# Optimization experiments

Hardware: AMD Instinct MI355X
Metric: run time of the kernel (lower is better)

The kernel has to match this reference:

```python
import jax, jax.numpy as jnp
import numpy as np

N_NODES = 50000
N_EDGES = 800000
DIM = 128
BN_EPS = 1e-5  # torch.nn.BatchNorm1d default


def _lin_init(k, fan_in, fan_out):
    kw, kb = jax.random.split(k)
    s = 1.0 / np.sqrt(fan_in)
    W = jax.random.uniform(kw, (fan_in, fan_out), jnp.float32, -s, s)
    b = jax.random.uniform(kb, (fan_out,), jnp.float32, -s, s)
    return W, b


def setup_inputs() -> dict:
    key = jax.random.key(0)
    ks = jax.random.split(key, 8)
    d = {}
    d['h'] = jax.random.normal(ks[0], (N_NODES, DIM), jnp.float32)
    d['e'] = jax.random.normal(ks[1], (N_EDGES, DIM), jnp.float32)
    d['src'] = jax.random.randint(ks[2], (N_EDGES,), 0, N_NODES)
    d['dst'] = jax.random.randint(ks[3], (N_EDGES,), 0, N_NODES)
    # mlp_atom: Linear(128,128) -> ReLU -> Linear(128,128)
    d['Wa1'], d['ba1'] = _lin_init(ks[4], DIM, DIM)
    d['Wa2'], d['ba2'] = _lin_init(ks[5], DIM, DIM)
    # mlp_bond
    d['Wb1'], d['bb1'] = _lin_init(ks[6], DIM, DIM)
    d['Wb2'], d['bb2'] = _lin_init(ks[7], DIM, DIM)
    # BatchNorm1d affine params
    d['gamma_a'] = jnp.ones((DIM,), jnp.float32)
    d['beta_a'] = jnp.zeros((DIM,), jnp.float32)
    d['gamma_b'] = jnp.ones((DIM,), jnp.float32)
    d['beta_b'] = jnp.zeros((DIM,), jnp.float32)
    return d


def _mlp(x, W1, b1, W2, b2):
    return jax.nn.relu(x @ W1 + b1) @ W2 + b2


def _bn(x, gamma, beta):
    # training-mode batch norm over the node/edge axis
    mu = jnp.mean(x, axis=0)
    var = jnp.var(x, axis=0)
    return (x - mu) * jax.lax.rsqrt(var + BN_EPS) * gamma + beta


def reference(h, e, src, dst, Wa1, ba1, Wa2, ba2, Wb1, bb1, Wb2, bb2,
              gamma_a, beta_a, gamma_b, beta_b):
    # --- bond (edge) update: GIN-style sum of endpoint atom feats + bond feat
    me = h[src] + h[dst] + e                      # [E, D] irregular gather
    e_new = _bn(_mlp(me, Wb1, bb1, Wb2, bb2), gamma_b, beta_b)
    e_new = e_new + e                             # residual (dropout=Identity)
    # --- atom (node) update: sum-aggregate incident bond feats
    agg = jax.ops.segment_sum(e_new, dst, num_segments=N_NODES)  # [N, D] scatter
    h_new = _bn(_mlp(h + agg, Wa1, ba1, Wa2, ba2), gamma_a, beta_a)
    h_new = h_new + h                             # residual
    return h_new, e_new
```

## Files before the change

### kernel.cpp

```cpp
#include <hip/hip_runtime.h>
#include <hip/hip_fp16.h>
#include <cstddef>

#define NN 50000
#define NE 800000
#define D 128
#define BN_EPS 1e-5f

typedef __attribute__((ext_vector_type(8))) short bf16x8;
typedef __attribute__((ext_vector_type(4))) float f32x4;
typedef __attribute__((ext_vector_type(4))) unsigned short us4;

__device__ __forceinline__ unsigned short f2bf(float x) {
    unsigned u = __float_as_uint(x);
    return (unsigned short)((u + 0x7fffu + ((u >> 16) & 1u)) >> 16);
}

__global__ __launch_bounds__(256) void wprep_kernel(
    const float* __restrict__ W, unsigned short* __restrict__ Wt)
{
    const int idx = blockIdx.x * 256 + threadIdx.x;
    const int j  = idx & 7;
    const int l  = (idx >> 3) & 63;
    const int ks = (idx >> 9) & 3;
    const int ct = (idx >> 11) & 7;
    const int n  = 16 * ct + (l & 15);
    const int k  = 32 * ks + ((l >> 4) << 3) + j;
    Wt[idx] = f2bf(W[k * 128 + n]);
}

template<int MODE, int HALFX>
__global__ __launch_bounds__(256, 2) void mlp_mfma_kernel(
    const float* __restrict__ h, const float* __restrict__ e_or_agg,
    const int* __restrict__ src, const int* __restrict__ dst,
    const unsigned short* __restrict__ Wt1, const float* __restrict__ b1,
    const unsigned short* __restrict__ Wt2, const float* __restrict__ b2,
    void* __restrict__ x2out_v, float* __restrict__ stats)
{
    __shared__ __align__(16) unsigned short Xh[8192];
    __shared__ __align__(16) float OUTB[64 * 132 + 2048];

    const int tid  = threadIdx.x;
    const int lane = tid & 63;
    const int w    = tid >> 6;
    const int cg   = tid & 31;
    const int rg   = tid >> 5;
    const int c0   = cg * 4;
    const long r0  = (long)blockIdx.x * 64;

    if (stats == (float*)1) OUTB[64 * 132 + (tid & 2047)] = 1.f;

    const bf16x8* Wg1 = (const bf16x8*)Wt1;
    bf16x8 wf[8][4];
#pragma unroll
    for (int ct = 0; ct < 8; ++ct)
#pragma unroll
        for (int ks = 0; ks < 4; ++ks)
            wf[ct][ks] = Wg1[(ct * 4 + ks) * 64 + lane];

#pragma unroll
    for (int p = 0; p < 8; ++p) {
        const int  row  = p * 8 + rg;
        const long grow = r0 + row;
        float4 v = make_float4(0.f, 0.f, 0.f, 0.f);
        if (MODE == 0) {
            const int sN = src[grow];
            const int dN = dst[grow];
            const float4 ev = *(const float4*)(e_or_agg + (size_t)grow * D + c0);
            const float4 hs = *(const float4*)(h + (size_t)sN * D + c0);
            const float4 hd = *(const float4*)(h + (size_t)dN * D + c0);
            v.x = ev.x + hs.x + hd.x; v.y = ev.y + hs.y + hd.y;
            v.z = ev.z + hs.z + hd.z; v.w = ev.w + hs.w + hd.w;
        } else {
            if (grow < NN) {
                const float4 hv = *(const float4*)(h + (size_t)grow * D + c0);
                const float4 av = *(const float4*)(e_or_agg + (size_t)grow * D + c0);
                v.x = hv.x + av.x; v.y = hv.y + av.y;
                v.z = hv.z + av.z; v.w = hv.w + av.w;
            }
        }
        us4 hi;
        hi.x = f2bf(v.x); hi.y = f2bf(v.y);
        hi.z = f2bf(v.z); hi.w = f2bf(v.w);
        const int addr = row * 128 + (((c0 >> 3) ^ (row & 7)) << 3) + (c0 & 7);
        *(us4*)&Xh[addr] = hi;
    }
    __syncthreads();

    const int arow = 16 * w + (lane & 15);
    bf16x8 ah[4];
#pragma unroll
    for (int ks = 0; ks < 4; ++ks) {
        const int col0  = 32 * ks + ((lane >> 4) << 3);
        const int aaddr = arow * 128 + (((col0 >> 3) ^ (arow & 7)) << 3);
        ah[ks] = *(const bf16x8*)&Xh[aaddr];
    }
    f32x4 acc[8];
#pragma unroll
    for (int ct = 0; ct < 8; ++ct) acc[ct] = (f32x4){0.f, 0.f, 0.f, 0.f};
#pragma unroll
    for (int ct = 0; ct < 8; ++ct)
#pragma unroll
        for (int ks = 0; ks < 4; ++ks)
            acc[ct] = __builtin_amdgcn_mfma_f32_16x16x32_bf16(ah[ks], wf[ct][ks], acc[ct], 0, 0, 0);

    const bf16x8* Wg2 = (const bf16x8*)Wt2;
#pragma unroll
    for (int ct = 0; ct < 8; ++ct)
#pragma unroll
        for (int ks = 0; ks < 4; ++ks)
            wf[ct][ks] = Wg2[(ct * 4 + ks) * 64 + lane];

#pragma unroll
    for (int ct = 0; ct < 8; ++ct) {
        const float b1c = b1[16 * ct + (lane & 15)];
#pragma unroll
        for (int r = 0; r < 4; ++r) {
            const int row = 16 * w + ((lane >> 4) << 2) + r;
            OUTB[row * 132 + 16 * ct + (lane & 15)] = fmaxf(acc[ct][r] + b1c, 0.f);
        }
    }
    __syncthreads();

#pragma unroll
    for (int p = 0; p < 8; ++p) {
        const int row = p * 8 + rg;
        const float4 v = *(const float4*)&OUTB[row * 132 + c0];
        us4 hi;
        hi.x = f2bf(v.x); hi.y = f2bf(v.y);
        hi.z = f2bf(v.z); hi.w = f2bf(v.w);
        const int addr = row * 128 + (((c0 >> 3) ^ (row & 7)) << 3) + (c0 & 7);
        *(us4*)&Xh[addr] = hi;
    }
    __syncthreads();

#pragma unroll
    for (int ks = 0; ks < 4; ++ks) {
        const int col0  = 32 * ks + ((lane >> 4) << 3);
        const int aaddr = arow * 128 + (((col0 >> 3) ^ (arow & 7)) << 3);
        ah[ks] = *(const bf16x8*)&Xh[aaddr];
    }
    f32x4 a2[8];
#pragma unroll
    for (int ct = 0; ct < 8; ++ct) a2[ct] = (f32x4){0.f, 0.f, 0.f, 0.f};
#pragma unroll
    for (int ct = 0; ct < 8; ++ct)
#pragma unroll
        for (int ks = 0; ks < 4; ++ks)
            a2[ct] = __builtin_amdgcn_mfma_f32_16x16x32_bf16(ah[ks], wf[ct][ks], a2[ct], 0, 0, 0);

#pragma unroll
    for (int ct = 0; ct < 8; ++ct) {
        const float b2c = b2[16 * ct + (lane & 15)];
#pragma unroll
        for (int r = 0; r < 4; ++r) {
            const int row = 16 * w + ((lane >> 4) << 2) + r;
            OUTB[row * 132 + 16 * ct + (lane & 15)] = a2[ct][r] + b2c;
        }
    }
    __syncthreads();

    float ts[4] = {0.f, 0.f, 0.f, 0.f};
    float tq[4] = {0.f, 0.f, 0.f, 0.f};
#pragma unroll
    for (int p = 0; p < 8; ++p) {
        const int  row  = p * 8 + rg;
        const long grow = r0 + row;
        if (MODE == 1 && grow >= NN) continue;
        const float4 v = *(const float4*)&OUTB[row * 132 + c0];
        if (HALFX) {
            const __half2 h0 = __floats2half2_rn(v.x, v.y);
            const __half2 h1 = __floats2half2_rn(v.z, v.w);
            int2 pk;
            pk.x = *(const int*)&h0;
            pk.y = *(const int*)&h1;
            *(int2*)((__half*)x2out_v + (size_t)grow * D + c0) = pk;
        } else {
            *(float4*)((float*)x2out_v + (size_t)grow * D + c0) = v;
        }
        ts[0] += v.x; ts[1] += v.y; ts[2] += v.z; ts[3] += v.w;
        tq[0] += v.x * v.x; tq[1] += v.y * v.y;
        tq[2] += v.z * v.z; tq[3] += v.w * v.w;
    }

    float* red = (float*)Xh;
    *(float4*)&red[rg * 128 + c0]        = make_float4(ts[0], ts[1], ts[2], ts[3]);
    *(float4*)&red[1024 + rg * 128 + c0] = make_float4(tq[0], tq[1], tq[2], tq[3]);
    __syncthreads();
    if (tid < 128) {
        float s = 0.f, q = 0.f;
#pragma unroll
        for (int g = 0; g < 8; ++g) {
            s += red[g * 128 + tid];
            q += red[1024 + g * 128 + tid];
        }
        unsafeAtomicAdd(&stats[tid], s);
        unsafeAtomicAdd(&stats[128 + tid], q);
    }
}

__global__ void bn_finalize_kernel(float* __restrict__ stats,
                                   const float* __restrict__ gamma,
                                   const float* __restrict__ beta,
                                   float inv_count)
{
    const int c = threadIdx.x;
    if (c < D) {
        const float mu  = stats[c] * inv_count;
        const float var = stats[128 + c] * inv_count - mu * mu;
        const float sc  = rsqrtf(var + BN_EPS) * gamma[c];
        stats[256 + c] = sc;
        stats[384 + c] = beta[c] - mu * sc;
    }
}

__global__ __launch_bounds__(256) void hist_kernel(
    const int* __restrict__ dst, int* __restrict__ cnt)
{
    const int i = blockIdx.x * 256 + threadIdx.x;
    if (i < NE) atomicAdd(&cnt[dst[i]], 1);
}

__global__ __launch_bounds__(1024) void scan_kernel(
    const int* __restrict__ cnt, int* __restrict__ off)
{
    __shared__ int part[1024];
    const int t = threadIdx.x;
    const int SEG = (NN + 1023) / 1024;
    const int base = t * SEG;

    int s = 0;
    for (int i = 0; i < SEG; ++i) {
        const int idx = base + i;
        if (idx < NN) s += cnt[idx];
    }
    part[t] = s;
    __syncthreads();
    for (int d = 1; d < 1024; d <<= 1) {
        int v = (t >= d) ? part[t - d] : 0;
        __syncthreads();
        part[t] += v;
        __syncthreads();
    }
    int run = (t > 0) ? part[t - 1] : 0;
    for (int i = 0; i < SEG; ++i) {
        const int idx = base + i;
        if (idx < NN) { off[idx] = run; run += cnt[idx]; }
    }
    if (t == 1023) off[NN] = part[1023];
}

__global__ __launch_bounds__(256) void csr_scatter_kernel(
    const int* __restrict__ dst, const int* __restrict__ off,
    int* __restrict__ cnt, int* __restrict__ csr)
{
    const int i = blockIdx.x * 256 + threadIdx.x;
    if (i < NE) {
        const int d = dst[i];
        const int p = atomicSub(&cnt[d], 1) - 1;
        csr[off[d] + p] = i;
    }
}

template<int HALFX>
__global__ __launch_bounds__(256) void apply_gather_kernel(
    const float* __restrict__ e, const float* __restrict__ stats,
    const int* __restrict__ off, const int* __restrict__ csr,
    const void* __restrict__ x2src, float* __restrict__ eout,
    float* __restrict__ agg)
{
    const int node = blockIdx.x * 4 + (threadIdx.x >> 6);
    const int lane = threadIdx.x & 63;
    const int half = lane >> 5;
    const int c0   = (lane & 31) * 4;
    if (node >= NN) return;

    const float4 sc = *(const float4*)(stats + 256 + c0);
    const float4 sh = *(const float4*)(stats + 384 + c0);
    float4 acc = make_float4(0.f, 0.f, 0.f, 0.f);
    const int jb = off[node], je = off[node + 1];
    const int niter = (je - jb + 1) >> 1;

#pragma unroll 2
    for (int p = 0; p < niter; ++p) {
        const int j0 = jb + 2 * p + half;
        if (j0 < je) {
            const int eidx = csr[j0];
            const size_t base = (size_t)eidx * D + c0;
            float4 x;
            if (HALFX) {
                const int2 xi = *(const int2*)((const __half*)x2src + base);
                const float2 f0 = __half22float2(*(const __half2*)&xi.x);
                const float2 f1 = __half22float2(*(const __half2*)&xi.y);
                x = make_float4(f0.x, f0.y, f1.x, f1.y);
            } else {
                x = *(const float4*)(eout + base);
            }
            const float4 ev = *(const float4*)(e + base);
            float4 v;
            v.x = fmaf(x.x, sc.x, sh.x) + ev.x;
            v.y = fmaf(x.y, sc.y, sh.y) + ev.y;
            v.z = fmaf(x.z, sc.z, sh.z) + ev.z;
            v.w = fmaf(x.w, sc.w, sh.w) + ev.w;
            *(float4*)(eout + base) = v;
            acc.x += v.x; acc.y += v.y; acc.z += v.z; acc.w += v.w;
        }
    }

    acc.x += __shfl_xor(acc.x, 32);
    acc.y += __shfl_xor(acc.y, 32);
    acc.z += __shfl_xor(acc.z, 32);
    acc.w += __shfl_xor(acc.w, 32);
    if (half == 0)
        *(float4*)(agg + (size_t)node * D + c0) = acc;
}

__global__ __launch_bounds__(256) void node_apply_kernel(
    const float* __restrict__ h, const float* __restrict__ stats,
    float* __restrict__ hout)
{
    const int gid = blockIdx.x * 256 + threadIdx.x;
    const int c0  = (gid & 31) * 4;
    const size_t base = (size_t)(gid >> 5) * D + c0;

    const float4 sc = *(const float4*)(stats + 256 + c0);
    const float4 sh = *(const float4*)(stats + 384 + c0);
    const float4 x  = *(const float4*)(hout + base);
    const float4 hv = *(const float4*)(h + base);
    float4 v;
    v.x = fmaf(x.x, sc.x, sh.x) + hv.x;
    v.y = fmaf(x.y, sc.y, sh.y) + hv.y;
    v.z = fmaf(x.z, sc.z, sh.z) + hv.z;
    v.w = fmaf(x.w, sc.w, sh.w) + hv.w;
    *(float4*)(hout + base) = v;
}

extern "C" void kernel_launch(void* const* d_in, const int* in_sizes, int n_in,
                              void* d_out, int out_size, void* d_ws, size_t ws_size,
                              hipStream_t stream)
{
    const float* h   = (const float*)d_in[0];
    const float* e   = (const float*)d_in[1];
    const int*   src = (const int*)d_in[2];
    const int*   dst = (const int*)d_in[3];
    const float* Wa1 = (const float*)d_in[4];
    const float* ba1 = (const float*)d_in[5];
    const float* Wa2 = (const float*)d_in[6];
    const float* ba2 = (const float*)d_in[7];
    const float* Wb1 = (const float*)d_in[8];
    const float* bb1 = (const float*)d_in[9];
    const float* Wb2 = (const float*)d_in[10];
    const float* bb2 = (const float*)d_in[11];
    const float* ga  = (const float*)d_in[12];
    const float* bea = (const float*)d_in[13];
    const float* gb  = (const float*)d_in[14];
    const float* beb = (const float*)d_in[15];

    float* out  = (float*)d_out;
    float* hnew = out;
    float* enew = out + (size_t)NN * D;

    float* ws     = (float*)d_ws;
    float* estats = ws;
    float* nstats = ws + 512;
    int*   icnt   = (int*)(ws + 1024);
    int*   ioff   = icnt + NN;
    unsigned short* wtb1 = (unsigned short*)(ioff + NN + 1 + 3);
    unsigned short* wtb2 = wtb1 + 16384;
    unsigned short* wta1 = wtb2 + 16384;
    unsigned short* wta2 = wta1 + 16384;
    int*    icsr = (int*)(wta2 + 16384);
    float*  agg  = (float*)(icsr + NE);
    __half* x2h  = (__half*)(agg + (size_t)NN * D);
    const size_t need_half = (size_t)((char*)(x2h + (size_t)NE * D) - (char*)d_ws);
    const bool use_half = (ws_size >= need_half);

    hipMemsetAsync(d_ws, 0, (size_t)(1024 + NN) * sizeof(float), stream);

    wprep_kernel<<<64, 256, 0, stream>>>(Wb1, wtb1);
    wprep_kernel<<<64, 256, 0, stream>>>(Wb2, wtb2);
    wprep_kernel<<<64, 256, 0, stream>>>(Wa1, wta1);
    wprep_kernel<<<64, 256, 0, stream>>>(Wa2, wta2);

    hist_kernel<<<(NE + 255) / 256, 256, 0, stream>>>(dst, icnt);
    scan_kernel<<<1, 1024, 0, stream>>>(icnt, ioff);
    csr_scatter_kernel<<<(NE + 255) / 256, 256, 0, stream>>>(dst, ioff, icnt, icsr);

    if (use_half) {
        mlp_mfma_kernel<0, 1><<<NE / 64, 256, 0, stream>>>(
            h, e, src, dst, wtb1, bb1, wtb2, bb2, (void*)x2h, estats);
        bn_finalize_kernel<<<1, 128, 0, stream>>>(estats, gb, beb, 1.0f / NE);
        apply_gather_kernel<1><<<(NN + 3) / 4, 256, 0, stream>>>(
            e, estats, ioff, icsr, (const void*)x2h, enew, agg);
    } else {
        mlp_mfma_kernel<0, 0><<<NE / 64, 256, 0, stream>>>(
            h, e, src, dst, wtb1, bb1, wtb2, bb2, (void*)enew, estats);
        bn_finalize_kernel<<<1, 128, 0, stream>>>(estats, gb, beb, 1.0f / NE);
        apply_gather_kernel<0><<<(NN + 3) / 4, 256, 0, stream>>>(
            e, estats, ioff, icsr, nullptr, enew, agg);
    }

    mlp_mfma_kernel<1, 0><<<(NN + 63) / 64, 256, 0, stream>>>(
        h, agg, nullptr, nullptr, wta1, ba1, wta2, ba2, (void*)hnew, nstats);
    bn_finalize_kernel<<<1, 128, 0, stream>>>(nstats, ga, bea, 1.0f / NN);
    node_apply_kernel<<<(NN * 32) / 256, 256, 0, stream>>>(h, nstats, hnew);
}
```

Before: 804.2 us.

## Split MLP column tiles across twice the waves per block, unroll gather loop further

The MLP kernel now runs 512 threads (8 waves) per 64-row tile. Each wave computes half of the 128 output columns, so it holds only half the weight fragments and accumulators. This lowers per-thread register pressure, allowing more waves per CU to hide gather latency. In exchange each wave reloads the A fragments redundantly and the stats reduction grows to 16 partials. The CSR gather loop unroll is also raised from 2 to 4.

```diff
diff --git a/kernel.cpp b/kernel.cpp
--- a/kernel.cpp
+++ b/kernel.cpp
@@ -30,7 +30,7 @@
 }
 
 template<int MODE, int HALFX>
-__global__ __launch_bounds__(256, 2) void mlp_mfma_kernel(
+__global__ __launch_bounds__(512, 4) void mlp_mfma_kernel(
     const float* __restrict__ h, const float* __restrict__ e_or_agg,
     const int* __restrict__ src, const int* __restrict__ dst,
     const unsigned short* __restrict__ Wt1, const float* __restrict__ b1,
@@ -43,6 +43,8 @@
     const int tid  = threadIdx.x;
     const int lane = tid & 63;
     const int w    = tid >> 6;
+    const int wq   = w & 3;
+    const int wh   = w >> 2;
     const int cg   = tid & 31;
     const int rg   = tid >> 5;
     const int c0   = cg * 4;
@@ -51,16 +53,16 @@
     if (stats == (float*)1) OUTB[64 * 132 + (tid & 2047)] = 1.f;
 
     const bf16x8* Wg1 = (const bf16x8*)Wt1;
-    bf16x8 wf[8][4];
-#pragma unroll
-    for (int ct = 0; ct < 8; ++ct)
+    bf16x8 wf[4][4];
+#pragma unroll
+    for (int ctl = 0; ctl < 4; ++ctl)
 #pragma unroll
         for (int ks = 0; ks < 4; ++ks)
-            wf[ct][ks] = Wg1[(ct * 4 + ks) * 64 + lane];
-
-#pragma unroll
-    for (int p = 0; p < 8; ++p) {
-        const int  row  = p * 8 + rg;
+            wf[ctl][ks] = Wg1[((4 * wh + ctl) * 4 + ks) * 64 + lane];
+
+#pragma unroll
+    for (int p = 0; p < 4; ++p) {
+        const int  row  = p * 16 + rg;
         const long grow = r0 + row;
         float4 v = make_float4(0.f, 0.f, 0.f, 0.f);
         if (MODE == 0) {
@@ -87,7 +89,7 @@
     }
     __syncthreads();
 
-    const int arow = 16 * w + (lane & 15);
+    const int arow = 16 * wq + (lane & 15);
     bf16x8 ah[4];
 #pragma unroll
     for (int ks = 0; ks < 4; ++ks) {
@@ -95,36 +97,37 @@
         const int aaddr = arow * 128 + (((col0 >> 3) ^ (arow & 7)) << 3);
         ah[ks] = *(const bf16x8*)&Xh[aaddr];
     }
-    f32x4 acc[8];
-#pragma unroll
-    for (int ct = 0; ct < 8; ++ct) acc[ct] = (f32x4){0.f, 0.f, 0.f, 0.f};
-#pragma unroll
-    for (int ct = 0; ct < 8; ++ct)
+    f32x4 acc[4];
+#pragma unroll
+    for (int ctl = 0; ctl < 4; ++ctl) acc[ctl] = (f32x4){0.f, 0.f, 0.f, 0.f};
+#pragma unroll
+    for (int ctl = 0; ctl < 4; ++ctl)
 #pragma unroll
         for (int ks = 0; ks < 4; ++ks)
-            acc[ct] = __builtin_amdgcn_mfma_f32_16x16x32_bf16(ah[ks], wf[ct][ks], acc[ct], 0, 0, 0);
+            acc[ctl] = __builtin_amdgcn_mfma_f32_16x16x32_bf16(ah[ks], wf[ctl][ks], acc[ctl], 0, 0, 0);
 
     const bf16x8* Wg2 = (const bf16x8*)Wt2;
 #pragma unroll
-    for (int ct = 0; ct < 8; ++ct)
+    for (int ctl = 0; ctl < 4; ++ctl)
 #pragma unroll
         for (int ks = 0; ks < 4; ++ks)
-            wf[ct][ks] = Wg2[(ct * 4 + ks) * 64 + lane];
-
-#pragma unroll
-    for (int ct = 0; ct < 8; ++ct) {
+            wf[ctl][ks] = Wg2[((4 * wh + ctl) * 4 + ks) * 64 + lane];
+
+#pragma unroll
+    for (int ctl = 0; ctl < 4; ++ctl) {
+        const int ct = 4 * wh + ctl;
         const float b1c = b1[16 * ct + (lane & 15)];
 #pragma unroll
         for (int r = 0; r < 4; ++r) {
-            const int row = 16 * w + ((lane >> 4) << 2) + r;
-            OUTB[row * 132 + 16 * ct + (lane & 15)] = fmaxf(acc[ct][r] + b1c, 0.f);
-        }
-    }
-    __syncthreads();
-
-#pragma unroll
-    for (int p = 0; p < 8; ++p) {
-        const int row = p * 8 + rg;
+            const int row = 16 * wq + ((lane >> 4) << 2) + r;
+            OUTB[row * 132 + 16 * ct + (lane & 15)] = fmaxf(acc[ctl][r] + b1c, 0.f);
+        }
+    }
+    __syncthreads();
+
+#pragma unroll
+    for (int p = 0; p < 4; ++p) {
+        const int row = p * 16 + rg;
         const float4 v = *(const float4*)&OUTB[row * 132 + c0];
         us4 hi;
         hi.x = f2bf(v.x); hi.y = f2bf(v.y);
@@ -140,22 +143,23 @@
         const int aaddr = arow * 128 + (((col0 >> 3) ^ (arow & 7)) << 3);
         ah[ks] = *(const bf16x8*)&Xh[aaddr];
     }
-    f32x4 a2[8];
-#pragma unroll
-    for (int ct = 0; ct < 8; ++ct) a2[ct] = (f32x4){0.f, 0.f, 0.f, 0.f};
-#pragma unroll
-    for (int ct = 0; ct < 8; ++ct)
+    f32x4 a2[4];
+#pragma unroll
+    for (int ctl = 0; ctl < 4; ++ctl) a2[ctl] = (f32x4){0.f, 0.f, 0.f, 0.f};
+#pragma unroll
+    for (int ctl = 0; ctl < 4; ++ctl)
 #pragma unroll
         for (int ks = 0; ks < 4; ++ks)
-            a2[ct] = __builtin_amdgcn_mfma_f32_16x16x32_bf16(ah[ks], wf[ct][ks], a2[ct], 0, 0, 0);
-
-#pragma unroll
-    for (int ct = 0; ct < 8; ++ct) {
+            a2[ctl] = __builtin_amdgcn_mfma_f32_16x16x32_bf16(ah[ks], wf[ctl][ks], a2[ctl], 0, 0, 0);
+
+#pragma unroll
+    for (int ctl = 0; ctl < 4; ++ctl) {
+        const int ct = 4 * wh + ctl;
         const float b2c = b2[16 * ct + (lane & 15)];
 #pragma unroll
         for (int r = 0; r < 4; ++r) {
-            const int row = 16 * w + ((lane >> 4) << 2) + r;
-            OUTB[row * 132 + 16 * ct + (lane & 15)] = a2[ct][r] + b2c;
+            const int row = 16 * wq + ((lane >> 4) << 2) + r;
+            OUTB[row * 132 + 16 * ct + (lane & 15)] = a2[ctl][r] + b2c;
         }
     }
     __syncthreads();
@@ -163,8 +167,8 @@
     float ts[4] = {0.f, 0.f, 0.f, 0.f};
     float tq[4] = {0.f, 0.f, 0.f, 0.f};
 #pragma unroll
-    for (int p = 0; p < 8; ++p) {
-        const int  row  = p * 8 + rg;
+    for (int p = 0; p < 4; ++p) {
+        const int  row  = p * 16 + rg;
         const long grow = r0 + row;
         if (MODE == 1 && grow >= NN) continue;
         const float4 v = *(const float4*)&OUTB[row * 132 + c0];
@@ -185,14 +189,14 @@
 
     float* red = (float*)Xh;
     *(float4*)&red[rg * 128 + c0]        = make_float4(ts[0], ts[1], ts[2], ts[3]);
-    *(float4*)&red[1024 + rg * 128 + c0] = make_float4(tq[0], tq[1], tq[2], tq[3]);
+    *(float4*)&red[2048 + rg * 128 + c0] = make_float4(tq[0], tq[1], tq[2], tq[3]);
     __syncthreads();
     if (tid < 128) {
         float s = 0.f, q = 0.f;
 #pragma unroll
-        for (int g = 0; g < 8; ++g) {
+        for (int g = 0; g < 16; ++g) {
             s += red[g * 128 + tid];
-            q += red[1024 + g * 128 + tid];
+            q += red[2048 + g * 128 + tid];
         }
         unsafeAtomicAdd(&stats[tid], s);
         unsafeAtomicAdd(&stats[128 + tid], q);
@@ -281,7 +285,7 @@
     const int jb = off[node], je = off[node + 1];
     const int niter = (je - jb + 1) >> 1;
 
-#pragma unroll 2
+#pragma unroll 4
     for (int p = 0; p < niter; ++p) {
         const int j0 = jb + 2 * p + half;
         if (j0 < je) {
@@ -387,20 +391,20 @@
     csr_scatter_kernel<<<(NE + 255) / 256, 256, 0, stream>>>(dst, ioff, icnt, icsr);
 
     if (use_half) {
-        mlp_mfma_kernel<0, 1><<<NE / 64, 256, 0, stream>>>(
+        mlp_mfma_kernel<0, 1><<<NE / 64, 512, 0, stream>>>(
             h, e, src, dst, wtb1, bb1, wtb2, bb2, (void*)x2h, estats);
         bn_finalize_kernel<<<1, 128, 0, stream>>>(estats, gb, beb, 1.0f / NE);
         apply_gather_kernel<1><<<(NN + 3) / 4, 256, 0, stream>>>(
             e, estats, ioff, icsr, (const void*)x2h, enew, agg);
     } else {
-        mlp_mfma_kernel<0, 0><<<NE / 64, 256, 0, stream>>>(
+        mlp_mfma_kernel<0, 0><<<NE / 64, 512, 0, stream>>>(
             h, e, src, dst, wtb1, bb1, wtb2, bb2, (void*)enew, estats);
         bn_finalize_kernel<<<1, 128, 0, stream>>>(estats, gb, beb, 1.0f / NE);
         apply_gather_kernel<0><<<(NN + 3) / 4, 256, 0, stream>>>(
             e, estats, ioff, icsr, nullptr, enew, agg);
     }
 
-    mlp_mfma_kernel<1, 0><<<(NN + 63) / 64, 256, 0, stream>>>(
+    mlp_mfma_kernel<1, 0><<<(NN + 63) / 64, 512, 0, stream>>>(
         h, agg, nullptr, nullptr, wta1, ba1, wta2, ba2, (void*)hnew, nstats);
     bn_finalize_kernel<<<1, 128, 0, stream>>>(nstats, ga, bea, 1.0f / NN);
     node_apply_kernel<<<(NN * 32) / 256, 256, 0, stream>>>(h, nstats, hnew);
```

After: 803.2 us. Within noise of the previous version (-0.1%).
